# Kernel tuning notes

Measured on AMD Instinct MI355X. Metric: run time of the kernel, lower is better.

Reference implementation:

```python
import jax, jax.numpy as jnp
import numpy as np

NLAYERS = 4
HEADS = 4
HEAD_DIM = 64
C = HEADS * HEAD_DIM  # 256
MAX_LEN = 1024


def setup_inputs() -> dict:
    key = jax.random.key(0)
    k1, k2, k3 = jax.random.split(key, 3)
    B, S = 16, 1024
    x = jax.random.normal(k1, (B, C, 1, S), dtype=jnp.float32)
    # length is only used via its static shape[0]; values are irrelevant
    length = jnp.zeros((MAX_LEN,), dtype=jnp.int32)
    # per-layer 1x1 conv weights, std=0.1 as in the torch init (squeeze the 1x1 spatial dims)
    w = jax.random.normal(k2, (NLAYERS, C, C), dtype=jnp.float32) * 0.1
    # persistent kv buffer
    kv = jax.random.normal(k3, (NLAYERS, HEADS, MAX_LEN, HEAD_DIM), dtype=jnp.float32) * 0.1
    return {"x": x, "length": length, "w": w, "kv": kv}


def reference(x, length, w, kv):
    B, _, _, S = x.shape
    L = length.shape[0]  # static slice length into kv buffer
    scale = 1.0 / jnp.sqrt(jnp.asarray(HEAD_DIM, dtype=x.dtype))
    for i in range(NLAYERS):
        # 1x1 conv == channel projection: (B,C,1,S) -> (B,C,1,S)
        x = jnp.einsum('oc,bchs->bohs', w[i], x)
        # view (B,4,64,S) then permute -> query (B,H,S,D)
        q = x.reshape(B, HEADS, HEAD_DIM, S).transpose(0, 1, 3, 2)
        kvi = kv[i, :, :L]  # (H, L, D); broadcasts over batch like the (1,H,L,D) torch slice
        # scaled dot-product attention with k == v == kvi
        scores = jnp.einsum('bhsd,hld->bhsl', q, kvi) * scale
        attn = jax.nn.softmax(scores, axis=-1)
        o = jnp.einsum('bhsl,hld->bhsd', attn, kvi)  # (B,H,S,D)
        # permute back and merge heads -> (B,256,1,S)
        x = o.transpose(0, 1, 3, 2).reshape(B, C, 1, S)
    return x
```

## Files before the change

### kernel.cpp

```cpp
#include <hip/hip_runtime.h>

#define NL   4
#define NH   4
#define HD   64
#define CD   256
#define SQL  1024
#define BB   16

typedef _Float16 half8 __attribute__((ext_vector_type(8)));
typedef _Float16 half4 __attribute__((ext_vector_type(4)));
typedef float    f32x4 __attribute__((ext_vector_type(4)));
typedef unsigned short u16x8 __attribute__((ext_vector_type(8)));

static __device__ __forceinline__ float bf2f(unsigned short u) {
    union { unsigned int i; float f; } v; v.i = ((unsigned int)u) << 16; return v.f;
}
static __device__ __forceinline__ unsigned short f2bf(float f) {
    union { float f; unsigned int i; } v; v.f = f;
    unsigned int u = v.i;
    return (unsigned short)((u + 0x7fffu + ((u >> 16) & 1u)) >> 16);
}

static __device__ __forceinline__ int detect_flag(const void* win) {
    const unsigned int* w = (const unsigned int*)win;
    int cnt = 0;
#pragma unroll 1
    for (int i = 0; i < 64; i++) {
        unsigned int lo = w[i] & 0xFFFFu;
        int e = (int)((lo >> 7) & 0xFF);
        cnt += (e >= 96 && e <= 144) ? 1 : 0;
    }
    return cnt >= 48 ? 1 : 0;
}

__global__ __launch_bounds__(256) void prep_all(const void* __restrict__ xin,
                                                const void* __restrict__ win,
                                                const void* __restrict__ kvin,
                                                _Float16* __restrict__ x16,
                                                _Float16* __restrict__ w16,
                                                _Float16* __restrict__ kv16,
                                                _Float16* __restrict__ kvT16) {
    __shared__ __align__(16) _Float16 tile[64][72];
    const int bi = blockIdx.x;
    const int t = threadIdx.x;
    const int isbf = detect_flag(win);

    if (bi < 1024) {
        const int st = bi & 15, ct = (bi >> 4) & 3, b = bi >> 6;
        const int r = t >> 2, seg = t & 3;
        const size_t base = ((size_t)(b * CD + ct * 64 + r)) * SQL + st * 64 + seg * 16;
        float v[16];
        if (isbf) {
            const unsigned short* src = (const unsigned short*)xin + base;
            u16x8 u0 = *(const u16x8*)(src);
            u16x8 u1 = *(const u16x8*)(src + 8);
#pragma unroll
            for (int j = 0; j < 8; j++) { v[j] = bf2f(u0[j]); v[8 + j] = bf2f(u1[j]); }
        } else {
            const float* src = (const float*)xin + base;
#pragma unroll
            for (int c = 0; c < 4; c++) {
                f32x4 a = *(const f32x4*)(src + c * 4);
#pragma unroll
                for (int j = 0; j < 4; j++) v[c * 4 + j] = a[j];
            }
        }
#pragma unroll
        for (int j = 0; j < 16; j++) tile[r][seg * 16 + j] = (_Float16)v[j];
        __syncthreads();
        half8 o0, o1;
#pragma unroll
        for (int j = 0; j < 8; j++) { o0[j] = tile[seg * 16 + j][r]; o1[j] = tile[seg * 16 + 8 + j][r]; }
        _Float16* dt = x16 + ((size_t)(b * SQL + st * 64 + r)) * CD + ct * 64 + seg * 16;
        *(half8*)(dt) = o0;
        *(half8*)(dt + 8) = o1;
    } else if (bi < 1280) {
        const int j2 = bi - 1024;
        const int lt = j2 & 15, ih = j2 >> 4;
        const int r = t >> 2, seg = t & 3;
        const size_t base = ((size_t)(ih * SQL + lt * 64 + r)) * HD + seg * 16;
        float v[16];
        if (isbf) {
            const unsigned short* src = (const unsigned short*)kvin + base;
            u16x8 u0 = *(const u16x8*)(src);
            u16x8 u1 = *(const u16x8*)(src + 8);
#pragma unroll
            for (int j = 0; j < 8; j++) { v[j] = bf2f(u0[j]); v[8 + j] = bf2f(u1[j]); }
        } else {
            const float* src = (const float*)kvin + base;
#pragma unroll
            for (int c = 0; c < 4; c++) {
                f32x4 a = *(const f32x4*)(src + c * 4);
#pragma unroll
                for (int j = 0; j < 4; j++) v[c * 4 + j] = a[j];
            }
        }
        half8 h0, h1;
#pragma unroll
        for (int j = 0; j < 8; j++) { h0[j] = (_Float16)v[j]; h1[j] = (_Float16)v[8 + j]; }
        _Float16* dst = kv16 + base;
        *(half8*)(dst) = h0;
        *(half8*)(dst + 8) = h1;
#pragma unroll
        for (int j = 0; j < 16; j++) tile[r][seg * 16 + j] = (_Float16)v[j];
        __syncthreads();
        half8 o0, o1;
#pragma unroll
        for (int j = 0; j < 8; j++) { o0[j] = tile[seg * 16 + j][r]; o1[j] = tile[seg * 16 + 8 + j][r]; }
        _Float16* dt = kvT16 + ((size_t)(ih * HD + r)) * SQL + lt * 64 + seg * 16;
        *(half8*)(dt) = o0;
        *(half8*)(dt + 8) = o1;
    } else {
        const int i = (bi - 1280) * 256 + t;
        const size_t base = (size_t)i * 8;
        half8 h;
        if (isbf) {
            u16x8 u = *(const u16x8*)((const unsigned short*)win + base);
#pragma unroll
            for (int j = 0; j < 8; j++) h[j] = (_Float16)bf2f(u[j]);
        } else {
            const float* p = (const float*)win + base;
            f32x4 a0 = *(const f32x4*)(p);
            f32x4 a1 = *(const f32x4*)(p + 4);
#pragma unroll
            for (int j = 0; j < 4; j++) { h[j] = (_Float16)a0[j]; h[4 + j] = (_Float16)a1[j]; }
        }
        *(half8*)(w16 + base) = h;
    }
}

__global__ __launch_bounds__(256) void layer_fused(const _Float16* __restrict__ xg,
                                                   _Float16* __restrict__ xout,
                                                   const _Float16* __restrict__ w16,
                                                   const _Float16* __restrict__ kv16,
                                                   const _Float16* __restrict__ kvT16,
                                                   const void* __restrict__ win,
                                                   void* __restrict__ outp,
                                                   int L) {
    __shared__ __align__(16) _Float16 kvl[2][4096];
    __shared__ __align__(16) _Float16 kvt[2][4096];
    const int sb = blockIdx.x;
    const int h  = blockIdx.y;
    const int b  = blockIdx.z;
    const int t  = threadIdx.x;
    const int wv = t >> 6, lane = t & 63, l16 = lane & 15, quad = lane >> 4;
    const int s0 = sb * 128 + wv * 32;

    const int cc = ((lane & 7) ^ (lane >> 3)) * 8;
    const size_t kvrow = ((size_t)(L * NH + h)) << 10;
    const size_t ktrow = ((size_t)(L * NH + h)) << 6;

    auto stage = [&](int lt) {
        const int buf = lt & 1;
#pragma unroll
        for (int rep = 0; rep < 2; rep++) {
            const int grp = wv * 2 + rep;
            const int R = grp * 8 + (lane >> 3);
            const _Float16* g0 = kv16 + ((kvrow + (lt << 6) + R) << 6) + cc;
            const _Float16* g1 = kvT16 + ((ktrow + R) << 10) + (lt << 6) + cc;
            __builtin_amdgcn_global_load_lds((const __attribute__((address_space(1))) void*)g0,
                (__attribute__((address_space(3))) void*)(&kvl[buf][grp * 512]), 16, 0, 0);
            __builtin_amdgcn_global_load_lds((const __attribute__((address_space(1))) void*)g1,
                (__attribute__((address_space(3))) void*)(&kvt[buf][grp * 512]), 16, 0, 0);
        }
    };
    stage(0);

    f32x4 gacc[4][2];
#pragma unroll
    for (int md = 0; md < 4; md++)
#pragma unroll
        for (int nt = 0; nt < 2; nt++)
#pragma unroll
            for (int r = 0; r < 4; r++) gacc[md][nt][r] = 0.0f;
    const _Float16* wb = w16 + ((size_t)L << 16) + ((size_t)(h * 64) << 8);
#pragma unroll
    for (int kk = 0; kk < 8; kk++) {
        half8 bx[2];
#pragma unroll
        for (int nt = 0; nt < 2; nt++)
            bx[nt] = *(const half8*)(xg + ((size_t)((b << 10) + s0 + nt * 16 + l16) << 8) +
                                     kk * 32 + quad * 8);
#pragma unroll
        for (int md = 0; md < 4; md++) {
            half8 aw = *(const half8*)(wb + ((size_t)(md * 16 + l16) << 8) + kk * 32 + quad * 8);
            gacc[md][0] = __builtin_amdgcn_mfma_f32_16x16x32_f16(aw, bx[0], gacc[md][0], 0, 0, 0);
            gacc[md][1] = __builtin_amdgcn_mfma_f32_16x16x32_f16(aw, bx[1], gacc[md][1], 0, 0, 0);
        }
    }
    half4 qh[4][2];
#pragma unroll
    for (int md = 0; md < 4; md++)
#pragma unroll
        for (int nt = 0; nt < 2; nt++)
#pragma unroll
            for (int r = 0; r < 4; r++)
                qh[md][nt][r] = (_Float16)(gacc[md][nt][r] * 0.180336880111120f);

    f32x4 oacc[4][2];
    float lsum[2] = {0.0f, 0.0f};
#pragma unroll
    for (int md = 0; md < 4; md++)
#pragma unroll
        for (int nt = 0; nt < 2; nt++)
#pragma unroll
            for (int r = 0; r < 4; r++) oacc[md][nt][r] = 0.0f;

    for (int lt = 0; lt < 16; lt++) {
        __syncthreads();
        if (lt + 1 < 16) stage(lt + 1);
        const _Float16* kl = kvl[lt & 1];
        const _Float16* kt = kvt[lt & 1];

        f32x4 stt[4][2];
#pragma unroll
        for (int ms = 0; ms < 4; ms++)
#pragma unroll
            for (int nt = 0; nt < 2; nt++)
#pragma unroll
                for (int r = 0; r < 4; r++) stt[ms][nt][r] = 0.0f;
#pragma unroll
        for (int kd = 0; kd < 4; kd++)
#pragma unroll
            for (int ms = 0; ms < 4; ms++) {
                half4 av = *(const half4*)(kl + (ms * 16 + l16) * 64 +
                           (((kd * 2 + (quad >> 1)) ^ (l16 & 7)) * 8) + (quad & 1) * 4);
#pragma unroll
                for (int nt = 0; nt < 2; nt++)
                    stt[ms][nt] = __builtin_amdgcn_mfma_f32_16x16x16f16(
                        av, qh[kd][nt], stt[ms][nt], 0, 0, 0);
            }

        half4 pb[4][2];
#pragma unroll
        for (int ms = 0; ms < 4; ms++)
#pragma unroll
            for (int nt = 0; nt < 2; nt++) {
                float e0 = __builtin_amdgcn_exp2f(stt[ms][nt][0]);
                float e1 = __builtin_amdgcn_exp2f(stt[ms][nt][1]);
                float e2 = __builtin_amdgcn_exp2f(stt[ms][nt][2]);
                float e3 = __builtin_amdgcn_exp2f(stt[ms][nt][3]);
                lsum[nt] += (e0 + e1) + (e2 + e3);
                half4 p; p[0] = (_Float16)e0; p[1] = (_Float16)e1;
                p[2] = (_Float16)e2; p[3] = (_Float16)e3;
                pb[ms][nt] = p;
            }

#pragma unroll
        for (int ks = 0; ks < 4; ks++)
#pragma unroll
            for (int md = 0; md < 4; md++) {
                half4 av = *(const half4*)(kt + (md * 16 + l16) * 64 +
                           (((ks * 2 + (quad >> 1)) ^ (l16 & 7)) * 8) + (quad & 1) * 4);
#pragma unroll
                for (int nt = 0; nt < 2; nt++)
                    oacc[md][nt] = __builtin_amdgcn_mfma_f32_16x16x16f16(
                        av, pb[ks][nt], oacc[md][nt], 0, 0, 0);
            }
    }

    float inv[2];
#pragma unroll
    for (int nt = 0; nt < 2; nt++) {
        float v = lsum[nt];
        v += __shfl_xor(v, 16);
        v += __shfl_xor(v, 32);
        inv[nt] = 1.0f / v;
    }

    if (L < NL - 1) {
#pragma unroll
        for (int md = 0; md < 4; md++)
#pragma unroll
            for (int nt = 0; nt < 2; nt++) {
                const int s = s0 + nt * 16 + l16;
                half4 hv;
#pragma unroll
                for (int r = 0; r < 4; r++) hv[r] = (_Float16)(oacc[md][nt][r] * inv[nt]);
                *(half4*)(xout + (((size_t)((b << 10) + s)) << 8) + (h << 6) + md * 16 + quad * 4) = hv;
            }
    } else if (detect_flag(win)) {
#pragma unroll
        for (int md = 0; md < 4; md++)
#pragma unroll
            for (int nt = 0; nt < 2; nt++) {
                const int s = s0 + nt * 16 + l16;
#pragma unroll
                for (int r = 0; r < 4; r++) {
                    const int c = (h << 6) + md * 16 + quad * 4 + r;
                    ((unsigned short*)outp)[(((size_t)(b * CD + c)) << 10) + s] =
                        f2bf(oacc[md][nt][r] * inv[nt]);
                }
            }
    } else {
#pragma unroll
        for (int md = 0; md < 4; md++)
#pragma unroll
            for (int nt = 0; nt < 2; nt++) {
                const int s = s0 + nt * 16 + l16;
#pragma unroll
                for (int r = 0; r < 4; r++) {
                    const int c = (h << 6) + md * 16 + quad * 4 + r;
                    ((float*)outp)[(((size_t)(b * CD + c)) << 10) + s] =
                        oacc[md][nt][r] * inv[nt];
                }
            }
    }
}

extern "C" void kernel_launch(void* const* d_in, const int* in_sizes, int n_in,
                              void* d_out, int out_size, void* d_ws, size_t ws_size,
                              hipStream_t stream) {
    const void* xin = d_in[0];
    const void* win = d_in[2];
    const void* kvin = d_in[3];

    char* ws = (char*)d_ws;
    const size_t MB = 1u << 20;
    _Float16* xa    = (_Float16*)(ws);
    _Float16* xb    = (_Float16*)(ws + 8 * MB);
    _Float16* w16   = (_Float16*)(ws + 16 * MB);
    _Float16* kv16  = (_Float16*)(ws + 17 * MB);
    _Float16* kvT16 = (_Float16*)(ws + 19 * MB);

    prep_all<<<dim3(1024 + 256 + 128), 256, 0, stream>>>(xin, win, kvin, xa, w16, kv16, kvT16);

    _Float16* cur = xa;
    _Float16* nxt = xb;
    for (int i = 0; i < NL; i++) {
        layer_fused<<<dim3(SQL / 128, NH, BB), 256, 0, stream>>>(cur, nxt, w16, kv16, kvT16,
                                                                 win, d_out, i);
        _Float16* tmp = cur; cur = nxt; nxt = tmp;
    }
}
```

Measured before the change: 249.1 us.

## Load KV tiles directly from global into registers instead of LDS staging

Removes the double-buffered LDS staging of K and V^T tiles (global_load_lds plus __syncthreads) and has each wave load its MFMA operands straight from global memory into registers, with the loop unrolled by two. This drops LDS traffic and block-wide barriers and may raise occupancy by freeing shared memory. In exchange, every wave fetches the same KV data redundantly through L1/L2, the loads are only 8-byte half4 per lane, and register pressure rises from holding 32 half4 operands.

```diff
diff --git a/kernel.cpp b/kernel.cpp
--- a/kernel.cpp
+++ b/kernel.cpp
@@ -137,8 +137,6 @@
                                                    const void* __restrict__ win,
                                                    void* __restrict__ outp,
                                                    int L) {
-    __shared__ __align__(16) _Float16 kvl[2][4096];
-    __shared__ __align__(16) _Float16 kvt[2][4096];
     const int sb = blockIdx.x;
     const int h  = blockIdx.y;
     const int b  = blockIdx.z;
@@ -146,26 +144,6 @@
     const int wv = t >> 6, lane = t & 63, l16 = lane & 15, quad = lane >> 4;
     const int s0 = sb * 128 + wv * 32;
 
-    const int cc = ((lane & 7) ^ (lane >> 3)) * 8;
-    const size_t kvrow = ((size_t)(L * NH + h)) << 10;
-    const size_t ktrow = ((size_t)(L * NH + h)) << 6;
-
-    auto stage = [&](int lt) {
-        const int buf = lt & 1;
-#pragma unroll
-        for (int rep = 0; rep < 2; rep++) {
-            const int grp = wv * 2 + rep;
-            const int R = grp * 8 + (lane >> 3);
-            const _Float16* g0 = kv16 + ((kvrow + (lt << 6) + R) << 6) + cc;
-            const _Float16* g1 = kvT16 + ((ktrow + R) << 10) + (lt << 6) + cc;
-            __builtin_amdgcn_global_load_lds((const __attribute__((address_space(1))) void*)g0,
-                (__attribute__((address_space(3))) void*)(&kvl[buf][grp * 512]), 16, 0, 0);
-            __builtin_amdgcn_global_load_lds((const __attribute__((address_space(1))) void*)g1,
-                (__attribute__((address_space(3))) void*)(&kvt[buf][grp * 512]), 16, 0, 0);
-        }
-    };
-    stage(0);
-
     f32x4 gacc[4][2];
 #pragma unroll
     for (int md = 0; md < 4; md++)
@@ -197,6 +175,9 @@
             for (int r = 0; r < 4; r++)
                 qh[md][nt][r] = (_Float16)(gacc[md][nt][r] * 0.180336880111120f);
 
+    const _Float16* kvh = kv16 + ((size_t)(L * NH + h) << 16);
+    const _Float16* kth = kvT16 + ((size_t)(L * NH + h) << 16);
+
     f32x4 oacc[4][2];
     float lsum[2] = {0.0f, 0.0f};
 #pragma unroll
@@ -206,11 +187,22 @@
 #pragma unroll
             for (int r = 0; r < 4; r++) oacc[md][nt][r] = 0.0f;
 
+#pragma unroll 2
     for (int lt = 0; lt < 16; lt++) {
-        __syncthreads();
-        if (lt + 1 < 16) stage(lt + 1);
-        const _Float16* kl = kvl[lt & 1];
-        const _Float16* kt = kvt[lt & 1];
+        half4 ka[4][4];
+#pragma unroll
+        for (int ms = 0; ms < 4; ms++)
+#pragma unroll
+            for (int kd = 0; kd < 4; kd++)
+                ka[ms][kd] = *(const half4*)(kvh + ((lt * 64 + ms * 16 + l16) << 6) +
+                                             kd * 16 + quad * 4);
+        half4 va[4][4];
+#pragma unroll
+        for (int md = 0; md < 4; md++)
+#pragma unroll
+            for (int ks = 0; ks < 4; ks++)
+                va[md][ks] = *(const half4*)(kth + ((md * 16 + l16) << 10) +
+                                             lt * 64 + ks * 16 + quad * 4);
 
         f32x4 stt[4][2];
 #pragma unroll
@@ -223,12 +215,10 @@
         for (int kd = 0; kd < 4; kd++)
 #pragma unroll
             for (int ms = 0; ms < 4; ms++) {
-                half4 av = *(const half4*)(kl + (ms * 16 + l16) * 64 +
-                           (((kd * 2 + (quad >> 1)) ^ (l16 & 7)) * 8) + (quad & 1) * 4);
 #pragma unroll
                 for (int nt = 0; nt < 2; nt++)
                     stt[ms][nt] = __builtin_amdgcn_mfma_f32_16x16x16f16(
-                        av, qh[kd][nt], stt[ms][nt], 0, 0, 0);
+                        ka[ms][kd], qh[kd][nt], stt[ms][nt], 0, 0, 0);
             }
 
         half4 pb[4][2];
@@ -250,12 +240,10 @@
         for (int ks = 0; ks < 4; ks++)
 #pragma unroll
             for (int md = 0; md < 4; md++) {
-                half4 av = *(const half4*)(kt + (md * 16 + l16) * 64 +
-                           (((ks * 2 + (quad >> 1)) ^ (l16 & 7)) * 8) + (quad & 1) * 4);
 #pragma unroll
                 for (int nt = 0; nt < 2; nt++)
                     oacc[md][nt] = __builtin_amdgcn_mfma_f32_16x16x16f16(
-                        av, pb[ks][nt], oacc[md][nt], 0, 0, 0);
+                        va[md][ks], pb[ks][nt], oacc[md][nt], 0, 0, 0);
             }
     }
 
```

After: 583.2 us. +134.1%, slower.
